# Performance work log

Hardware: AMD Instinct MI355X
Metric: run time of the kernel (lower is better)

The kernel has to match this reference:

```python
import jax, jax.numpy as jnp
import numpy as np
import math

NUM_EXPERTS = 8
MIN_EXPERTS_ACTIVE = 2  # max(1, 8 // 4) per __init__ formula


def setup_inputs() -> dict:
    key = jax.random.key(0)
    ks = jax.random.split(key, 6)
    N, Cin, H, W = 16384, 68, 8, 8
    Cproj = 128
    patch = jax.random.normal(ks[0], (N, Cin, H, W), dtype=jnp.float32)
    conv_w = jax.random.normal(ks[1], (Cproj, Cin, 3, 3), dtype=jnp.float32) * (1.0 / np.sqrt(Cin * 9))
    conv_b = jnp.zeros((Cproj,), dtype=jnp.float32)
    fc_w = jax.random.normal(ks[2], (Cproj, NUM_EXPERTS), dtype=jnp.float32) * (1.0 / np.sqrt(Cproj))
    fc_b = jnp.zeros((NUM_EXPERTS,), dtype=jnp.float32)
    wth_max_c = jnp.float32(0.4)
    wth_entropy_c = jnp.float32(0.3)
    wth_gap_c = jnp.float32(0.3)
    threshold = jnp.float32(0.2)
    return {
        'patch': patch, 'conv_w': conv_w, 'conv_b': conv_b,
        'fc_w': fc_w, 'fc_b': fc_b,
        'wth_max_c': wth_max_c, 'wth_entropy_c': wth_entropy_c, 'wth_gap_c': wth_gap_c,
        'threshold': threshold, 'layer_idx': 0, 'current_epoch': 30,
    }


def _gate(patch, conv_w, conv_b, fc_w, fc_b):
    # 3x3 SAME conv (NCHW) -> ReLU -> global avg pool -> linear
    y = jax.lax.conv_general_dilated(
        patch, conv_w, window_strides=(1, 1), padding='SAME',
        dimension_numbers=('NCHW', 'OIHW', 'NCHW'))
    y = jax.nn.relu(y + conv_b[None, :, None, None])
    pooled = y.mean(axis=(2, 3))  # [N, Cproj]
    return pooled @ fc_w + fc_b   # [N, E]


def _compute_gap(sw):
    # sw: [N, E] sorted descending
    k = min(4, NUM_EXPERTS - 1)
    mean_rest = sw[:, 1:k + 1].mean(axis=-1, keepdims=True)
    gap = (sw[:, 0:1] - mean_rest) / (sw[:, 0:1] + 1e-8)
    return jnp.clip(gap, 0.0, 1.0)


def _adaptive_threshold(w, base_threshold, wth_max_c, wth_entropy_c, wth_gap_c):
    sw = -jnp.sort(-w, axis=-1)  # descending
    max_component = 1.0 - sw[:, 0:1]
    mean_w = w.mean(axis=-1, keepdims=True)
    std_w = w.std(axis=-1, keepdims=True, ddof=1)  # torch default unbiased
    entropy = -(w * jnp.log(w + 1e-18)).sum(axis=-1, keepdims=True)
    entropy_component = 1.0 - entropy / math.log(NUM_EXPERTS)
    gap_component = _compute_gap(sw)
    adaptive_factor = (wth_max_c * max_component + wth_entropy_c * entropy_component
                       + wth_gap_c * gap_component)
    th = base_threshold * (0.5 + adaptive_factor)
    min_th = jnp.maximum(jnp.float32(0.05), mean_w - 0.5 * std_w)
    max_th = jnp.minimum(jnp.float32(0.7), sw[:, 0:1] - 0.1 * std_w)
    th = jnp.clip(th, min_th, max_th)
    kth = sw[:, MIN_EXPERTS_ACTIVE - 1:MIN_EXPERTS_ACTIVE]
    return jnp.minimum(th, kth * 0.9)


def reference(patch, conv_w, conv_b, fc_w, fc_b,
              wth_max_c, wth_entropy_c, wth_gap_c,
              threshold, layer_idx, current_epoch):
    logits = _gate(patch, conv_w, conv_b, fc_w, fc_b)
    weights = jax.nn.softmax(logits, axis=-1)
    th = _adaptive_threshold(weights, threshold, wth_max_c, wth_entropy_c, wth_gap_c)
    if current_epoch is not None and current_epoch < 20:
        weights_norm = jnp.ones_like(weights) / NUM_EXPERTS
    elif current_epoch is not None and 20 <= current_epoch <= 25:
        tau = max(0.1, 1.0 - (current_epoch - 20) * 0.18)
        s = jax.nn.sigmoid((weights - th) / tau)
        weights_norm = s / jnp.clip(s.sum(axis=-1, keepdims=True), 1e-8)
    else:  # current_epoch > 25 or eval: straight-through hard/soft masking
        tau = 0.1
        hard = (weights > th).astype(weights.dtype)
        soft = jax.nn.sigmoid((weights - th) / tau)
        filtered = hard + jax.lax.stop_gradient(soft - hard)
        weights_norm = filtered / jnp.clip(filtered.sum(axis=-1, keepdims=True), 1e-8)
    return weights_norm
```

## Files before the change

kernel.cpp:

```cpp
#include <hip/hip_runtime.h>


typedef _Float16 half8 __attribute__((ext_vector_type(8)));
typedef float    floatx4 __attribute__((ext_vector_type(4)));

#define A_SAMPLE  14400
#define LDS_P_OFF 57600
#define LDS_TOTAL 59648

__global__ void prep_weights(const float* __restrict__ cw, _Float16* __restrict__ Bw) {
  int i = blockIdx.x * 256 + threadIdx.x;
  int co = i / 672;
  int k  = i - co * 672;
  int s  = k / 72;
  int ci = k - s * 72;
  float v = 0.f;
  if (s < 9 && ci < 68) {
    int ky = s / 3, kx = s - 3 * ky;
    v = cw[((co * 68 + ci) * 3 + ky) * 3 + kx];
  }
  Bw[i] = (_Float16)v;
}

__global__ __launch_bounds__(256, 2) void router_main(
    const float* __restrict__ patch,
    const float* __restrict__ conv_b,
    const _Float16* __restrict__ Bw,
    const float* __restrict__ fc_w,
    const float* __restrict__ fc_b,
    const float* __restrict__ p_wmax,
    const float* __restrict__ p_went,
    const float* __restrict__ p_wgap,
    const float* __restrict__ p_thr,
    const int* __restrict__ p_epoch,
    float* __restrict__ out)
{
  __shared__ __align__(16) unsigned char lds[LDS_TOTAL];
  const int tid    = threadIdx.x;
  const int l      = tid & 63;
  const int w      = tid >> 6;
  const int lane15 = l & 15;
  const int quad   = l >> 4;
  const int m_half = w >> 1;
  const int n0     = (w & 1) * 64;
  const int n_s    = blockIdx.x * 4;

  {
    unsigned char* abase = lds + w * A_SAMPLE;
    float4 z4 = make_float4(0.f, 0.f, 0.f, 0.f);
    #pragma unroll
    for (int j = 0; j < 15; ++j) {
      int idx = j * 64 + l;
      if (idx < 900) *(float4*)(abase + idx * 16) = z4;
    }
  }
  {
    const float* psrc = patch + (size_t)(n_s + w) * 4352 + l;
    int y = l >> 3, x = l & 7;
    unsigned char* arow = lds + w * A_SAMPLE + ((y + 1) * 10 + (x + 1)) * 144;
    #pragma unroll
    for (int b = 0; b < 9; ++b) {
      half8 h;
      #pragma unroll
      for (int j = 0; j < 8; ++j) {
        int ci = b * 8 + j;
        float v = (ci < 68) ? psrc[ci * 64] : 0.f;
        h[j] = (_Float16)v;
      }
      *(half8*)(arow + b * 16) = h;
    }
  }
  __syncthreads();

  int apos[8];
  #pragma unroll
  for (int t = 0; t < 8; ++t) {
    int p  = (t & 3) * 16 + lane15;
    int pp = ((p >> 3) + 1) * 10 + (p & 7) + 1;
    apos[t] = (m_half * 2 + (t >> 2)) * A_SAMPLE + pp * 144;
  }

  const _Float16* bptr[4];
  #pragma unroll
  for (int n = 0; n < 4; ++n)
    bptr[n] = Bw + (size_t)(n0 + n * 16 + lane15) * 672 + quad * 8;

  floatx4 acc[8][4];
  floatx4 zacc = {0.f, 0.f, 0.f, 0.f};
  #pragma unroll
  for (int t = 0; t < 8; ++t)
    #pragma unroll
    for (int n = 0; n < 4; ++n) acc[t][n] = zacc;

  half8 bcur[4];
  #pragma unroll
  for (int n = 0; n < 4; ++n) bcur[n] = *(const half8*)(bptr[n]);

  #pragma unroll 4
  for (int c = 0; c < 20; ++c) {
    half8 bnext[4];
    #pragma unroll
    for (int n = 0; n < 4; ++n)
      bnext[n] = *(const half8*)(bptr[n] + (c + 1) * 32);

    int kb  = c * 4 + quad;
    int s   = (kb * 57) >> 9;
    int rem = kb - s * 9;
    int dy  = (s * 11) >> 5;
    int dx  = s - 3 * dy;
    int roff = (dy * 10 + dx - 11) * 144 + rem * 16;

    half8 afr[8];
    #pragma unroll
    for (int t = 0; t < 8; ++t)
      afr[t] = *(const half8*)(lds + apos[t] + roff);

    #pragma unroll
    for (int t = 0; t < 8; ++t)
      #pragma unroll
      for (int n = 0; n < 4; ++n)
        acc[t][n] = __builtin_amdgcn_mfma_f32_16x16x32_f16(afr[t], bcur[n], acc[t][n], 0, 0, 0);

    #pragma unroll
    for (int n = 0; n < 4; ++n) bcur[n] = bnext[n];
  }

  {
    int roff = (quad == 0) ? 1712 : 0;
    half8 afr[8];
    #pragma unroll
    for (int t = 0; t < 8; ++t)
      afr[t] = *(const half8*)(lds + apos[t] + roff);
    #pragma unroll
    for (int t = 0; t < 8; ++t)
      #pragma unroll
      for (int n = 0; n < 4; ++n)
        acc[t][n] = __builtin_amdgcn_mfma_f32_16x16x32_f16(afr[t], bcur[n], acc[t][n], 0, 0, 0);
  }

  float bcoef[4];
  #pragma unroll
  for (int n = 0; n < 4; ++n) bcoef[n] = conv_b[n0 + n * 16 + lane15];

  float* pl = (float*)(lds + LDS_P_OFF);
  #pragma unroll
  for (int gl = 0; gl < 2; ++gl) {
    #pragma unroll
    for (int n = 0; n < 4; ++n) {
      float ssum = 0.f;
      #pragma unroll
      for (int tt = 0; tt < 4; ++tt) {
        int t = gl * 4 + tt;
        #pragma unroll
        for (int r = 0; r < 4; ++r)
          ssum += fmaxf(acc[t][n][r] + bcoef[n], 0.f);
      }
      ssum += __shfl_xor(ssum, 16);
      ssum += __shfl_xor(ssum, 32);
      if (l < 16) {
        int g = m_half * 2 + gl;
        pl[g * 128 + n0 + n * 16 + lane15] = ssum * (1.f / 64.f);
      }
    }
  }
  __syncthreads();

  const float* plw = pl + w * 128;
  int e  = l >> 3;
  int c8 = l & 7;
  float part = 0.f;
  #pragma unroll
  for (int m = 0; m < 16; ++m) {
    int co = c8 + 8 * m;
    part += plw[co] * fc_w[co * 8 + e];
  }
  part += __shfl_xor(part, 1);
  part += __shfl_xor(part, 2);
  part += __shfl_xor(part, 4);

  float lg[8];
  #pragma unroll
  for (int j = 0; j < 8; ++j) lg[j] = __shfl(part, j * 8) + fc_b[j];

  float mx = lg[0];
  #pragma unroll
  for (int j = 1; j < 8; ++j) mx = fmaxf(mx, lg[j]);
  float wgt[8]; float sum = 0.f;
  #pragma unroll
  for (int j = 0; j < 8; ++j) { wgt[j] = expf(lg[j] - mx); sum += wgt[j]; }
  float inv = 1.f / sum;
  #pragma unroll
  for (int j = 0; j < 8; ++j) wgt[j] *= inv;

  float sw[8];
  #pragma unroll
  for (int j = 0; j < 8; ++j) sw[j] = wgt[j];
  #define CSD(i, j) { float hi_ = fmaxf(sw[i], sw[j]); float lo_ = fminf(sw[i], sw[j]); sw[i] = hi_; sw[j] = lo_; }
  CSD(0,1) CSD(2,3) CSD(4,5) CSD(6,7)
  CSD(0,2) CSD(1,3) CSD(4,6) CSD(5,7)
  CSD(1,2) CSD(5,6)
  CSD(0,4) CSD(1,5) CSD(2,6) CSD(3,7)
  CSD(2,4) CSD(3,5)
  CSD(1,2) CSD(3,4) CSD(5,6)
  #undef CSD

  float s1 = 0.f;
  #pragma unroll
  for (int j = 0; j < 8; ++j) s1 += wgt[j];
  float mean = s1 * 0.125f;
  float var = 0.f;
  #pragma unroll
  for (int j = 0; j < 8; ++j) { float d = wgt[j] - mean; var += d * d; }
  float stdv = sqrtf(var * (1.f / 7.f));
  float ent = 0.f;
  #pragma unroll
  for (int j = 0; j < 8; ++j) ent -= wgt[j] * logf(wgt[j] + 1e-18f);

  float maxc  = 1.f - sw[0];
  float entc  = 1.f - ent * 0.48089834696298783f;
  float mrest = (sw[1] + sw[2] + sw[3] + sw[4]) * 0.25f;
  float gap   = (sw[0] - mrest) / (sw[0] + 1e-8f);
  gap = fminf(fmaxf(gap, 0.f), 1.f);
  float af = p_wmax[0] * maxc + p_went[0] * entc + p_wgap[0] * gap;
  float th = p_thr[0] * (0.5f + af);
  float mn  = fmaxf(0.05f, mean - 0.5f * stdv);
  float mxt = fminf(0.7f, sw[0] - 0.1f * stdv);
  th = fminf(fmaxf(th, mn), mxt);
  th = fminf(th, sw[1] * 0.9f);

  int epoch = p_epoch[0];
  float outv[8];
  if (epoch < 20) {
    #pragma unroll
    for (int j = 0; j < 8; ++j) outv[j] = 0.125f;
  } else {
    float tau = (epoch <= 25) ? fmaxf(0.1f, 1.0f - (float)(epoch - 20) * 0.18f) : 0.1f;
    float ssum = 0.f;
    #pragma unroll
    for (int j = 0; j < 8; ++j) {
      float sj = 1.f / (1.f + expf(-(wgt[j] - th) / tau));
      outv[j] = sj; ssum += sj;
    }
    float invs = 1.f / fmaxf(ssum, 1e-8f);
    #pragma unroll
    for (int j = 0; j < 8; ++j) outv[j] *= invs;
  }

  if (l < 8) {
    float mv = outv[0];
    #pragma unroll
    for (int j = 1; j < 8; ++j) mv = (l == j) ? outv[j] : mv;
    out[(n_s + w) * 8 + l] = mv;
  }
}

extern "C" void kernel_launch(void* const* d_in, const int* in_sizes, int n_in,
                              void* d_out, int out_size, void* d_ws, size_t ws_size,
                              hipStream_t stream) {
  const float* patch  = (const float*)d_in[0];
  const float* conv_w = (const float*)d_in[1];
  const float* conv_b = (const float*)d_in[2];
  const float* fc_w   = (const float*)d_in[3];
  const float* fc_b   = (const float*)d_in[4];
  const float* wmax   = (const float*)d_in[5];
  const float* went   = (const float*)d_in[6];
  const float* wgap   = (const float*)d_in[7];
  const float* thr    = (const float*)d_in[8];
  const int*   epoch  = (const int*)d_in[10];
  float* outp = (float*)d_out;
  _Float16* Bw = (_Float16*)d_ws;

  int N = in_sizes[0] / 4352;
  prep_weights<<<336, 256, 0, stream>>>(conv_w, Bw);
  router_main<<<N / 4, 256, 0, stream>>>(patch, conv_b, Bw, fc_w, fc_b,
                                         wmax, went, wgap, thr, epoch, outp);
}
```

Baseline: 491.8 us.

## Process two samples per block to cut LDS and registers and raise occupancy

Each block now handles two samples instead of four. Each wave computes one sample's half of the output channels, which halves the accumulator registers and the LDS footprint and raises the launch bound from 2 to 5 blocks per CU. Zeroing is limited to the padding border rows, and the patch load is split between the two waves assigned to a sample. In exchange, each B-weight fragment fetched from global memory feeds fewer MFMAs, so weight reloads per sample double, and only two of the four waves run the epilogue.

```diff
diff --git a/kernel.cpp b/kernel.cpp
--- a/kernel.cpp
+++ b/kernel.cpp
@@ -5,8 +5,8 @@
 typedef float    floatx4 __attribute__((ext_vector_type(4)));
 
 #define A_SAMPLE  14400
-#define LDS_P_OFF 57600
-#define LDS_TOTAL 59648
+#define LDS_P_OFF 28800
+#define LDS_TOTAL 29824
 
 __global__ void prep_weights(const float* __restrict__ cw, _Float16* __restrict__ Bw) {
   int i = blockIdx.x * 256 + threadIdx.x;
@@ -22,7 +22,7 @@
   Bw[i] = (_Float16)v;
 }
 
-__global__ __launch_bounds__(256, 2) void router_main(
+__global__ __launch_bounds__(256, 5) void router_main(
     const float* __restrict__ patch,
     const float* __restrict__ conv_b,
     const _Float16* __restrict__ Bw,
@@ -41,43 +41,55 @@
   const int w      = tid >> 6;
   const int lane15 = l & 15;
   const int quad   = l >> 4;
-  const int m_half = w >> 1;
-  const int n0     = (w & 1) * 64;
-  const int n_s    = blockIdx.x * 4;
+  const int sm     = w >> 1;
+  const int h      = w & 1;
+  const int n0     = h * 64;
+  const int n_s    = blockIdx.x * 2;
 
   {
-    unsigned char* abase = lds + w * A_SAMPLE;
+    unsigned char* abase = lds + sm * A_SAMPLE;
     float4 z4 = make_float4(0.f, 0.f, 0.f, 0.f);
     #pragma unroll
-    for (int j = 0; j < 15; ++j) {
-      int idx = j * 64 + l;
-      if (idx < 900) *(float4*)(abase + idx * 16) = z4;
+    for (int j0 = 0; j0 < 3; ++j0) {
+      int jj = j0 * 64 + l;
+      if (jj < 162) {
+        int j   = h * 162 + jj;
+        int ri  = j / 9;
+        int col = j - ri * 9;
+        int row = (ri < 10) ? ri
+                : (ri < 26) ? ((((ri - 10) >> 1) + 1) * 10 + ((ri - 10) & 1) * 9)
+                            : (ri + 64);
+        *(float4*)(abase + row * 144 + col * 16) = z4;
+      }
     }
   }
   {
-    const float* psrc = patch + (size_t)(n_s + w) * 4352 + l;
+    const float* psrc = patch + (size_t)(n_s + sm) * 4352 + l;
     int y = l >> 3, x = l & 7;
-    unsigned char* arow = lds + w * A_SAMPLE + ((y + 1) * 10 + (x + 1)) * 144;
-    #pragma unroll
-    for (int b = 0; b < 9; ++b) {
-      half8 h;
-      #pragma unroll
-      for (int j = 0; j < 8; ++j) {
-        int ci = b * 8 + j;
-        float v = (ci < 68) ? psrc[ci * 64] : 0.f;
-        h[j] = (_Float16)v;
+    unsigned char* arow = lds + sm * A_SAMPLE + ((y + 1) * 10 + (x + 1)) * 144;
+    #pragma unroll
+    for (int bb = 0; bb < 5; ++bb) {
+      int b = bb * 2 + h;
+      if (b < 9) {
+        half8 hh;
+        #pragma unroll
+        for (int j = 0; j < 8; ++j) {
+          int ci = b * 8 + j;
+          float v = (ci < 68) ? psrc[ci * 64] : 0.f;
+          hh[j] = (_Float16)v;
+        }
+        *(half8*)(arow + b * 16) = hh;
       }
-      *(half8*)(arow + b * 16) = h;
     }
   }
   __syncthreads();
 
-  int apos[8];
-  #pragma unroll
-  for (int t = 0; t < 8; ++t) {
-    int p  = (t & 3) * 16 + lane15;
+  int apos[4];
+  #pragma unroll
+  for (int t = 0; t < 4; ++t) {
+    int p  = t * 16 + lane15;
     int pp = ((p >> 3) + 1) * 10 + (p & 7) + 1;
-    apos[t] = (m_half * 2 + (t >> 2)) * A_SAMPLE + pp * 144;
+    apos[t] = sm * A_SAMPLE + pp * 144;
   }
 
   const _Float16* bptr[4];
@@ -85,10 +97,10 @@
   for (int n = 0; n < 4; ++n)
     bptr[n] = Bw + (size_t)(n0 + n * 16 + lane15) * 672 + quad * 8;
 
-  floatx4 acc[8][4];
+  floatx4 acc[4][4];
   floatx4 zacc = {0.f, 0.f, 0.f, 0.f};
   #pragma unroll
-  for (int t = 0; t < 8; ++t)
+  for (int t = 0; t < 4; ++t)
     #pragma unroll
     for (int n = 0; n < 4; ++n) acc[t][n] = zacc;
 
@@ -110,13 +122,13 @@
     int dx  = s - 3 * dy;
     int roff = (dy * 10 + dx - 11) * 144 + rem * 16;
 
-    half8 afr[8];
-    #pragma unroll
-    for (int t = 0; t < 8; ++t)
+    half8 afr[4];
+    #pragma unroll
+    for (int t = 0; t < 4; ++t)
       afr[t] = *(const half8*)(lds + apos[t] + roff);
 
     #pragma unroll
-    for (int t = 0; t < 8; ++t)
+    for (int t = 0; t < 4; ++t)
       #pragma unroll
       for (int n = 0; n < 4; ++n)
         acc[t][n] = __builtin_amdgcn_mfma_f32_16x16x32_f16(afr[t], bcur[n], acc[t][n], 0, 0, 0);
@@ -127,12 +139,12 @@
 
   {
     int roff = (quad == 0) ? 1712 : 0;
-    half8 afr[8];
-    #pragma unroll
-    for (int t = 0; t < 8; ++t)
+    half8 afr[4];
+    #pragma unroll
+    for (int t = 0; t < 4; ++t)
       afr[t] = *(const half8*)(lds + apos[t] + roff);
     #pragma unroll
-    for (int t = 0; t < 8; ++t)
+    for (int t = 0; t < 4; ++t)
       #pragma unroll
       for (int n = 0; n < 4; ++n)
         acc[t][n] = __builtin_amdgcn_mfma_f32_16x16x32_f16(afr[t], bcur[n], acc[t][n], 0, 0, 0);
@@ -144,113 +156,108 @@
 
   float* pl = (float*)(lds + LDS_P_OFF);
   #pragma unroll
-  for (int gl = 0; gl < 2; ++gl) {
-    #pragma unroll
-    for (int n = 0; n < 4; ++n) {
+  for (int n = 0; n < 4; ++n) {
+    float ssum = 0.f;
+    #pragma unroll
+    for (int t = 0; t < 4; ++t)
+      #pragma unroll
+      for (int r = 0; r < 4; ++r)
+        ssum += fmaxf(acc[t][n][r] + bcoef[n], 0.f);
+    ssum += __shfl_xor(ssum, 16);
+    ssum += __shfl_xor(ssum, 32);
+    if (l < 16)
+      pl[sm * 128 + n0 + n * 16 + lane15] = ssum * (1.f / 64.f);
+  }
+  __syncthreads();
+
+  if (w < 2) {
+    const float* plw = pl + w * 128;
+    int e  = l >> 3;
+    int c8 = l & 7;
+    float part = 0.f;
+    #pragma unroll
+    for (int m = 0; m < 16; ++m) {
+      int co = c8 + 8 * m;
+      part += plw[co] * fc_w[co * 8 + e];
+    }
+    part += __shfl_xor(part, 1);
+    part += __shfl_xor(part, 2);
+    part += __shfl_xor(part, 4);
+
+    float lg[8];
+    #pragma unroll
+    for (int j = 0; j < 8; ++j) lg[j] = __shfl(part, j * 8) + fc_b[j];
+
+    float mx = lg[0];
+    #pragma unroll
+    for (int j = 1; j < 8; ++j) mx = fmaxf(mx, lg[j]);
+    float wgt[8]; float sum = 0.f;
+    #pragma unroll
+    for (int j = 0; j < 8; ++j) { wgt[j] = expf(lg[j] - mx); sum += wgt[j]; }
+    float inv = 1.f / sum;
+    #pragma unroll
+    for (int j = 0; j < 8; ++j) wgt[j] *= inv;
+
+    float sw[8];
+    #pragma unroll
+    for (int j = 0; j < 8; ++j) sw[j] = wgt[j];
+    #define CSD(i, j) { float hi_ = fmaxf(sw[i], sw[j]); float lo_ = fminf(sw[i], sw[j]); sw[i] = hi_; sw[j] = lo_; }
+    CSD(0,1) CSD(2,3) CSD(4,5) CSD(6,7)
+    CSD(0,2) CSD(1,3) CSD(4,6) CSD(5,7)
+    CSD(1,2) CSD(5,6)
+    CSD(0,4) CSD(1,5) CSD(2,6) CSD(3,7)
+    CSD(2,4) CSD(3,5)
+    CSD(1,2) CSD(3,4) CSD(5,6)
+    #undef CSD
+
+    float s1 = 0.f;
+    #pragma unroll
+    for (int j = 0; j < 8; ++j) s1 += wgt[j];
+    float mean = s1 * 0.125f;
+    float var = 0.f;
+    #pragma unroll
+    for (int j = 0; j < 8; ++j) { float d = wgt[j] - mean; var += d * d; }
+    float stdv = sqrtf(var * (1.f / 7.f));
+    float ent = 0.f;
+    #pragma unroll
+    for (int j = 0; j < 8; ++j) ent -= wgt[j] * logf(wgt[j] + 1e-18f);
+
+    float maxc  = 1.f - sw[0];
+    float entc  = 1.f - ent * 0.48089834696298783f;
+    float mrest = (sw[1] + sw[2] + sw[3] + sw[4]) * 0.25f;
+    float gap   = (sw[0] - mrest) / (sw[0] + 1e-8f);
+    gap = fminf(fmaxf(gap, 0.f), 1.f);
+    float af = p_wmax[0] * maxc + p_went[0] * entc + p_wgap[0] * gap;
+    float th = p_thr[0] * (0.5f + af);
+    float mn  = fmaxf(0.05f, mean - 0.5f * stdv);
+    float mxt = fminf(0.7f, sw[0] - 0.1f * stdv);
+    th = fminf(fmaxf(th, mn), mxt);
+    th = fminf(th, sw[1] * 0.9f);
+
+    int epoch = p_epoch[0];
+    float outv[8];
+    if (epoch < 20) {
+      #pragma unroll
+      for (int j = 0; j < 8; ++j) outv[j] = 0.125f;
+    } else {
+      float tau = (epoch <= 25) ? fmaxf(0.1f, 1.0f - (float)(epoch - 20) * 0.18f) : 0.1f;
       float ssum = 0.f;
       #pragma unroll
-      for (int tt = 0; tt < 4; ++tt) {
-        int t = gl * 4 + tt;
-        #pragma unroll
-        for (int r = 0; r < 4; ++r)
-          ssum += fmaxf(acc[t][n][r] + bcoef[n], 0.f);
+      for (int j = 0; j < 8; ++j) {
+        float sj = 1.f / (1.f + expf(-(wgt[j] - th) / tau));
+        outv[j] = sj; ssum += sj;
       }
-      ssum += __shfl_xor(ssum, 16);
-      ssum += __shfl_xor(ssum, 32);
-      if (l < 16) {
-        int g = m_half * 2 + gl;
-        pl[g * 128 + n0 + n * 16 + lane15] = ssum * (1.f / 64.f);
-      }
-    }
-  }
-  __syncthreads();
-
-  const float* plw = pl + w * 128;
-  int e  = l >> 3;
-  int c8 = l & 7;
-  float part = 0.f;
-  #pragma unroll
-  for (int m = 0; m < 16; ++m) {
-    int co = c8 + 8 * m;
-    part += plw[co] * fc_w[co * 8 + e];
-  }
-  part += __shfl_xor(part, 1);
-  part += __shfl_xor(part, 2);
-  part += __shfl_xor(part, 4);
-
-  float lg[8];
-  #pragma unroll
-  for (int j = 0; j < 8; ++j) lg[j] = __shfl(part, j * 8) + fc_b[j];
-
-  float mx = lg[0];
-  #pragma unroll
-  for (int j = 1; j < 8; ++j) mx = fmaxf(mx, lg[j]);
-  float wgt[8]; float sum = 0.f;
-  #pragma unroll
-  for (int j = 0; j < 8; ++j) { wgt[j] = expf(lg[j] - mx); sum += wgt[j]; }
-  float inv = 1.f / sum;
-  #pragma unroll
-  for (int j = 0; j < 8; ++j) wgt[j] *= inv;
-
-  float sw[8];
-  #pragma unroll
-  for (int j = 0; j < 8; ++j) sw[j] = wgt[j];
-  #define CSD(i, j) { float hi_ = fmaxf(sw[i], sw[j]); float lo_ = fminf(sw[i], sw[j]); sw[i] = hi_; sw[j] = lo_; }
-  CSD(0,1) CSD(2,3) CSD(4,5) CSD(6,7)
-  CSD(0,2) CSD(1,3) CSD(4,6) CSD(5,7)
-  CSD(1,2) CSD(5,6)
-  CSD(0,4) CSD(1,5) CSD(2,6) CSD(3,7)
-  CSD(2,4) CSD(3,5)
-  CSD(1,2) CSD(3,4) CSD(5,6)
-  #undef CSD
-
-  float s1 = 0.f;
-  #pragma unroll
-  for (int j = 0; j < 8; ++j) s1 += wgt[j];
-  float mean = s1 * 0.125f;
-  float var = 0.f;
-  #pragma unroll
-  for (int j = 0; j < 8; ++j) { float d = wgt[j] - mean; var += d * d; }
-  float stdv = sqrtf(var * (1.f / 7.f));
-  float ent = 0.f;
-  #pragma unroll
-  for (int j = 0; j < 8; ++j) ent -= wgt[j] * logf(wgt[j] + 1e-18f);
-
-  float maxc  = 1.f - sw[0];
-  float entc  = 1.f - ent * 0.48089834696298783f;
-  float mrest = (sw[1] + sw[2] + sw[3] + sw[4]) * 0.25f;
-  float gap   = (sw[0] - mrest) / (sw[0] + 1e-8f);
-  gap = fminf(fmaxf(gap, 0.f), 1.f);
-  float af = p_wmax[0] * maxc + p_went[0] * entc + p_wgap[0] * gap;
-  float th = p_thr[0] * (0.5f + af);
-  float mn  = fmaxf(0.05f, mean - 0.5f * stdv);
-  float mxt = fminf(0.7f, sw[0] - 0.1f * stdv);
-  th = fminf(fmaxf(th, mn), mxt);
-  th = fminf(th, sw[1] * 0.9f);
-
-  int epoch = p_epoch[0];
-  float outv[8];
-  if (epoch < 20) {
-    #pragma unroll
-    for (int j = 0; j < 8; ++j) outv[j] = 0.125f;
-  } else {
-    float tau = (epoch <= 25) ? fmaxf(0.1f, 1.0f - (float)(epoch - 20) * 0.18f) : 0.1f;
-    float ssum = 0.f;
-    #pragma unroll
-    for (int j = 0; j < 8; ++j) {
-      float sj = 1.f / (1.f + expf(-(wgt[j] - th) / tau));
-      outv[j] = sj; ssum += sj;
-    }
-    float invs = 1.f / fmaxf(ssum, 1e-8f);
-    #pragma unroll
-    for (int j = 0; j < 8; ++j) outv[j] *= invs;
-  }
-
-  if (l < 8) {
-    float mv = outv[0];
-    #pragma unroll
-    for (int j = 1; j < 8; ++j) mv = (l == j) ? outv[j] : mv;
-    out[(n_s + w) * 8 + l] = mv;
+      float invs = 1.f / fmaxf(ssum, 1e-8f);
+      #pragma unroll
+      for (int j = 0; j < 8; ++j) outv[j] *= invs;
+    }
+
+    if (l < 8) {
+      float mv = outv[0];
+      #pragma unroll
+      for (int j = 1; j < 8; ++j) mv = (l == j) ? outv[j] : mv;
+      out[(n_s + w) * 8 + l] = mv;
+    }
   }
 }
 
@@ -272,6 +279,6 @@
 
   int N = in_sizes[0] / 4352;
   prep_weights<<<336, 256, 0, stream>>>(conv_w, Bw);
-  router_main<<<N / 4, 256, 0, stream>>>(patch, conv_b, Bw, fc_w, fc_b,
+  router_main<<<N / 2, 256, 0, stream>>>(patch, conv_b, Bw, fc_w, fc_b,
                                          wmax, went, wgap, thr, epoch, outp);
 }
```

Result: slower. 1.359 ms (+176.3%).

## Reorder LDS activation layout by channel block and pre-swizzle weights for coalesced loads

Applied to the files above, without the earlier changes.

The padded activation tile in LDS moves from a pixel-major layout (144-byte stride per pixel) to a channel-block-major layout (1600-byte planes, 16-byte stride per pixel). Only the halo border is zeroed instead of the whole tile. The weight prep kernel now writes fp16 weights in the exact per-lane, per-chunk order the MFMA loop reads, so each lane's B loads are contiguous 64-byte runs. This targets LDS bank conflicts on A-fragment reads, shortens zero-init work, and makes global B loads coalesced, at the cost of more complex index arithmetic.

```diff
diff --git a/kernel.cpp b/kernel.cpp
--- a/kernel.cpp
+++ b/kernel.cpp
@@ -9,15 +9,25 @@
 #define LDS_TOTAL 59648
 
 __global__ void prep_weights(const float* __restrict__ cw, _Float16* __restrict__ Bw) {
-  int i = blockIdx.x * 256 + threadIdx.x;
-  int co = i / 672;
-  int k  = i - co * 672;
-  int s  = k / 72;
-  int ci = k - s * 72;
+  int i  = blockIdx.x * 256 + threadIdx.x;
+  int h  = (i >= 43008) ? 1 : 0;
+  int r1 = i - h * 43008;
+  int c  = r1 >> 11;
+  int r2 = r1 & 2047;
+  int l  = r2 >> 5;
+  int r3 = r2 & 31;
+  int n  = r3 >> 3;
+  int j  = r3 & 7;
+  int quad = l >> 4, lane15 = l & 15;
+  int col  = h * 64 + n * 16 + lane15;
+  int kdim = (c * 4 + quad) * 8 + j;
+  int kb   = kdim >> 3;
+  int s    = (kb * 57) >> 9;
+  int ci   = kdim - s * 72;
   float v = 0.f;
   if (s < 9 && ci < 68) {
     int ky = s / 3, kx = s - 3 * ky;
-    v = cw[((co * 68 + ci) * 3 + ky) * 3 + kx];
+    v = cw[((col * 68 + ci) * 3 + ky) * 3 + kx];
   }
   Bw[i] = (_Float16)v;
 }
@@ -43,31 +53,39 @@
   const int quad   = l >> 4;
   const int m_half = w >> 1;
   const int n0     = (w & 1) * 64;
+  const int h      = w & 1;
   const int n_s    = blockIdx.x * 4;
 
   {
     unsigned char* abase = lds + w * A_SAMPLE;
     float4 z4 = make_float4(0.f, 0.f, 0.f, 0.f);
     #pragma unroll
-    for (int j = 0; j < 15; ++j) {
-      int idx = j * 64 + l;
-      if (idx < 900) *(float4*)(abase + idx * 16) = z4;
+    for (int j0 = 0; j0 < 6; ++j0) {
+      int j = j0 * 64 + l;
+      if (j < 324) {
+        int rem = (j * 57) >> 11;
+        int e   = j - rem * 36;
+        int pp = (e < 10) ? e
+               : (e < 20) ? (80 + e)
+               : ((((e - 20) >> 1) + 1) * 10 + ((e - 20) & 1) * 9);
+        *(float4*)(abase + (rem * 100 + pp) * 16) = z4;
+      }
     }
   }
   {
     const float* psrc = patch + (size_t)(n_s + w) * 4352 + l;
     int y = l >> 3, x = l & 7;
-    unsigned char* arow = lds + w * A_SAMPLE + ((y + 1) * 10 + (x + 1)) * 144;
+    unsigned char* abase = lds + w * A_SAMPLE + ((y + 1) * 10 + (x + 1)) * 16;
     #pragma unroll
     for (int b = 0; b < 9; ++b) {
-      half8 h;
+      half8 hh;
       #pragma unroll
       for (int j = 0; j < 8; ++j) {
         int ci = b * 8 + j;
         float v = (ci < 68) ? psrc[ci * 64] : 0.f;
-        h[j] = (_Float16)v;
-      }
-      *(half8*)(arow + b * 16) = h;
+        hh[j] = (_Float16)v;
+      }
+      *(half8*)(abase + b * 1600) = hh;
     }
   }
   __syncthreads();
@@ -77,13 +95,10 @@
   for (int t = 0; t < 8; ++t) {
     int p  = (t & 3) * 16 + lane15;
     int pp = ((p >> 3) + 1) * 10 + (p & 7) + 1;
-    apos[t] = (m_half * 2 + (t >> 2)) * A_SAMPLE + pp * 144;
-  }
-
-  const _Float16* bptr[4];
-  #pragma unroll
-  for (int n = 0; n < 4; ++n)
-    bptr[n] = Bw + (size_t)(n0 + n * 16 + lane15) * 672 + quad * 8;
+    apos[t] = (m_half * 2 + (t >> 2)) * A_SAMPLE + pp * 16;
+  }
+
+  const _Float16* bb = Bw + h * 43008 + l * 32;
 
   floatx4 acc[8][4];
   floatx4 zacc = {0.f, 0.f, 0.f, 0.f};
@@ -94,21 +109,21 @@
 
   half8 bcur[4];
   #pragma unroll
-  for (int n = 0; n < 4; ++n) bcur[n] = *(const half8*)(bptr[n]);
+  for (int n = 0; n < 4; ++n) bcur[n] = *(const half8*)(bb + n * 8);
 
   #pragma unroll 4
   for (int c = 0; c < 20; ++c) {
     half8 bnext[4];
     #pragma unroll
     for (int n = 0; n < 4; ++n)
-      bnext[n] = *(const half8*)(bptr[n] + (c + 1) * 32);
+      bnext[n] = *(const half8*)(bb + (c + 1) * 2048 + n * 8);
 
     int kb  = c * 4 + quad;
     int s   = (kb * 57) >> 9;
     int rem = kb - s * 9;
     int dy  = (s * 11) >> 5;
     int dx  = s - 3 * dy;
-    int roff = (dy * 10 + dx - 11) * 144 + rem * 16;
+    int roff = rem * 1600 + (dy * 10 + dx - 11) * 16;
 
     half8 afr[8];
     #pragma unroll
@@ -126,7 +141,7 @@
   }
 
   {
-    int roff = (quad == 0) ? 1712 : 0;
+    int roff = (quad == 0) ? 12976 : 0;
     half8 afr[8];
     #pragma unroll
     for (int t = 0; t < 8; ++t)
```

Measured after the change: 495.8 us. Within noise of the previous version (+0.8%).
